# Optimization experiments

Hardware: AMD Instinct MI355X
Metric: run time of the kernel (lower is better)

## Reference

```python
import jax, jax.numpy as jnp
import numpy as np

N = 65536      # num ref nodes
M = 65536      # num query nodes
E = 1572864    # num edges (avg degree 24)
K0 = 27        # num kernels (3x3x3 neighborhood)
D1 = 64        # input channels
D2 = 64        # output channels


def setup_inputs() -> dict:
    key = jax.random.key(0)
    k1, k2, k3, k4, k5, k6 = jax.random.split(key, 6)
    # kernel init mirrors initialize_kernel_weight (uniform in [-bound, bound])
    fan_in = D1 * K0
    gain = float(np.sqrt(2.0 / (1.0 + 5.0)))  # leaky_relu gain with slope sqrt(5)
    std = gain / np.sqrt(fan_in)
    bound = float(np.sqrt(3.0) * std)
    kernel = jax.random.uniform(k1, (K0, D1, D2), minval=-bound, maxval=bound, dtype=jnp.float32)
    ref_feat = jax.random.normal(k2, (N, D1), dtype=jnp.float32)
    e_kernel = jax.random.randint(k3, (E,), 0, K0)
    e_ref = jax.random.randint(k4, (E,), 0, N)
    e_query = jax.random.randint(k5, (E,), 0, M)
    e_weight = jax.random.uniform(k6, (E,), dtype=jnp.float32)
    return {
        "kernel": kernel,
        "ref_feat": ref_feat,
        "e_kernel": e_kernel,
        "e_ref": e_ref,
        "e_query": e_query,
        "num_queries": M,
        "e_weight": e_weight,
    }


def reference(kernel, ref_feat, e_kernel, e_ref, e_query, num_queries, e_weight):
    # Math of MessagePassing.forward:
    #   query_feat[m] = sum_{edges e: e_query[e]==m} w_e * (ref_feat[e_ref[e]] @ kernel[e_kernel[e]])
    # Efficient form: precompute each node's transform under every kernel
    # (N*K0*D1*D2 dense GEMM), then gather per edge and scatter-reduce.
    transformed = jnp.einsum('nd,kdo->nko', ref_feat, kernel)   # [N, K0, D2]
    msgs = transformed[e_ref, e_kernel] * e_weight[:, None]      # [E, D2]
    query_feat = jax.ops.segment_sum(msgs, e_query, num_segments=num_queries)  # [M, D2]
    return query_feat
```

## Files before the change

### kernel.cpp

```cpp
#include <hip/hip_runtime.h>

#define DIN 64
#define DOUT 64
#define MAXK 32

typedef __bf16 bf16x8 __attribute__((ext_vector_type(8)));
typedef float  f32x4  __attribute__((ext_vector_type(4)));
typedef unsigned int u32x4 __attribute__((ext_vector_type(4)));

static __device__ inline unsigned short f2b(float x) {
    return __builtin_bit_cast(unsigned short, (__bf16)x);
}
static __device__ inline float b2f(unsigned short u) {
    return __uint_as_float(((unsigned int)u) << 16);
}


__global__ void conv_w_kernel(const float* __restrict__ W,
                              unsigned short* __restrict__ Wt, int total,
                              int* __restrict__ qcount, int NB) {
    int i = blockIdx.x * blockDim.x + threadIdx.x;
    if (i < NB) qcount[i] = 0;
    if (i < total) {
        int j    = i & 7;
        int lane = (i >> 3) & 63;
        int h    = (i >> 9) & 1;
        int t    = (i >> 10) & 3;
        int k    = i >> 12;
        int col  = lane & 15;
        int quad = lane >> 4;
        int d1 = h * 32 + quad * 8 + j;
        int d2 = t * 16 + col;
        Wt[i] = f2b(W[(k * 64 + d1) * 64 + d2]);
    }
}


#define KSPLIT 8

__global__ __launch_bounds__(256) void phaseA_v3_kernel(
    const float* __restrict__ ref,
    const unsigned short* __restrict__ Wt,
    unsigned short* __restrict__ T,
    int K0, int Nn)
{
    const int lane = threadIdx.x & 63;
    const int wid  = threadIdx.x >> 6;
    const int col  = lane & 15;
    const int quad = lane >> 4;
    const int n0   = blockIdx.x * 64 + wid * 16;
    const int row  = n0 + col;

    const int kch = (K0 + KSPLIT - 1) / KSPLIT;
    const int k0  = blockIdx.y * kch;
    int k1 = k0 + kch;
    if (k1 > K0) k1 = K0;

    __shared__ __align__(16) char ldsbuf[4 * 2 * 2304];
    char* bufs = ldsbuf + wid * 2 * 2304;

    const float* rp = ref + (size_t)row * 64;
    f32x4 r0 = *reinterpret_cast<const f32x4*>(rp + quad * 8);
    f32x4 r1 = *reinterpret_cast<const f32x4*>(rp + quad * 8 + 4);
    f32x4 r2 = *reinterpret_cast<const f32x4*>(rp + 32 + quad * 8);
    f32x4 r3 = *reinterpret_cast<const f32x4*>(rp + 32 + quad * 8 + 4);
    bf16x8 b0, b1;
    #pragma unroll
    for (int i = 0; i < 4; ++i) {
        b0[i]     = (__bf16)r0[i];
        b0[4 + i] = (__bf16)r1[i];
        b1[i]     = (__bf16)r2[i];
        b1[4 + i] = (__bf16)r3[i];
    }

    const int rrow = lane >> 2;
    const int rq   = lane & 3;

    for (int k = k0; k < k1; ++k) {
        char* buf = bufs + (k & 1) * 2304;
        const unsigned short* Wk = Wt + (size_t)k * 4096;
        #pragma unroll
        for (int t = 0; t < 4; ++t) {
            const unsigned short* ap = Wk + (size_t)t * 1024 + lane * 8;
            bf16x8 a0 = *reinterpret_cast<const bf16x8*>(ap);
            bf16x8 a1 = *reinterpret_cast<const bf16x8*>(ap + 512);
            f32x4 c = {0.f, 0.f, 0.f, 0.f};
            c = __builtin_amdgcn_mfma_f32_16x16x32_bf16(a0, b0, c, 0, 0, 0);
            c = __builtin_amdgcn_mfma_f32_16x16x32_bf16(a1, b1, c, 0, 0, 0);
            unsigned int lo = (unsigned int)f2b(c[0]) | ((unsigned int)f2b(c[1]) << 16);
            unsigned int hi = (unsigned int)f2b(c[2]) | ((unsigned int)f2b(c[3]) << 16);
            *reinterpret_cast<uint2*>(buf + col * 144 + t * 32 + quad * 8) =
                make_uint2(lo, hi);
        }
        u32x4 v0 = *reinterpret_cast<const u32x4*>(buf + rrow * 144 + rq * 32);
        u32x4 v1 = *reinterpret_cast<const u32x4*>(buf + rrow * 144 + rq * 32 + 16);
        size_t gbase = ((size_t)k * Nn + n0 + rrow) * 64 + rq * 16;
        *reinterpret_cast<u32x4*>(T + gbase)     = v0;
        *reinterpret_cast<u32x4*>(T + gbase + 8) = v1;
    }
}


__global__ void p1_hist_kernel(const int* __restrict__ eq, int E,
                               int* __restrict__ qcount) {
    __shared__ int l[1024];
    const int t = threadIdx.x;
    #pragma unroll
    for (int s4 = 0; s4 < 4; ++s4) l[t + s4 * 256] = 0;
    __syncthreads();
    int stride = gridDim.x * blockDim.x;
    for (int i = blockIdx.x * blockDim.x + t; i < E; i += stride)
        atomicAdd(&l[((unsigned)eq[i]) >> 6], 1);
    __syncthreads();
    #pragma unroll
    for (int s4 = 0; s4 < 4; ++s4) {
        int v = l[t + s4 * 256];
        if (v) atomicAdd(&qcount[t + s4 * 256], v);
    }
}

__global__ void p1_scan_kernel(const int* __restrict__ qcount,
                               int* __restrict__ gbase, int* __restrict__ gcursor,
                               int* __restrict__ qstart, int NB, int M, int E) {
    __shared__ int sh[1024];
    int t = threadIdx.x;
    int v = (t < NB) ? qcount[t] : 0;
    sh[t] = v;
    __syncthreads();
    #pragma unroll
    for (int o = 1; o < 1024; o <<= 1) {
        int x = (t >= o) ? sh[t - o] : 0;
        __syncthreads();
        sh[t] += x;
        __syncthreads();
    }
    int ex = sh[t] - v;
    if (t < NB) { gbase[t] = ex; gcursor[t] = ex; }
    if (t == 0) qstart[M] = E;
}

__global__ __launch_bounds__(256) void p1_scatter_kernel(
    const int* __restrict__ eq, const int* __restrict__ er,
    const int* __restrict__ ek, const float* __restrict__ ew,
    int E, int* __restrict__ gcursor, uint2* __restrict__ tmp)
{
    __shared__ int bin[1024];
    __shared__ int base[1024];
    const int t = threadIdx.x;
    #pragma unroll
    for (int s4 = 0; s4 < 4; ++s4) bin[t + s4 * 256] = 0;
    __syncthreads();
    const int i0 = blockIdx.x * 4096;
    unsigned key[16];
    unsigned rank[16];
    uint2 pay[16];
    #pragma unroll
    for (int u = 0; u < 16; ++u) {
        int i = i0 + u * 256 + t;
        if (i < E) {
            int q = eq[i];
            unsigned b = ((unsigned)q) >> 6;
            key[u] = b;
            rank[u] = atomicAdd(&bin[b], 1);
            pay[u] = make_uint2((unsigned)er[i] | ((unsigned)ek[i] << 16) |
                                ((unsigned)(q & 63) << 21),
                                __float_as_uint(ew[i]));
        } else {
            key[u] = 0xFFFFFFFFu;
        }
    }
    __syncthreads();
    #pragma unroll
    for (int s4 = 0; s4 < 4; ++s4) {
        int bb = t + s4 * 256;
        int c = bin[bb];
        if (c) base[bb] = atomicAdd(&gcursor[bb], c);
    }
    __syncthreads();
    #pragma unroll
    for (int u = 0; u < 16; ++u) {
        if (key[u] != 0xFFFFFFFFu)
            tmp[(size_t)base[key[u]] + rank[u]] = pay[u];
    }
}

__global__ __launch_bounds__(256) void p2_kernel(
    const uint2* __restrict__ tmp, const int* __restrict__ gbase,
    const int* __restrict__ qcount, uint2* __restrict__ rec,
    int* __restrict__ qstart)
{
    __shared__ int fine[64];
    __shared__ int foff[64];
    const int b = blockIdx.x;
    const int t = threadIdx.x;
    const int s = gbase[b];
    const int L = qcount[b];
    if (t < 64) fine[t] = 0;
    __syncthreads();
    for (int i = t; i < L; i += 256)
        atomicAdd(&fine[(tmp[s + i].x >> 21) & 63], 1);
    __syncthreads();
    if (t < 64) {
        int v = fine[t];
        int x = v;
        #pragma unroll
        for (int o = 1; o < 64; o <<= 1) {
            int y = __shfl_up(x, o);
            if (t >= o) x += y;
        }
        foff[t] = x - v;
        qstart[b * 64 + t] = s + x - v;
        fine[t] = 0;
    }
    __syncthreads();
    for (int i = t; i < L; i += 256) {
        uint2 p = tmp[s + i];
        unsigned fb = (p.x >> 21) & 63;
        int r = atomicAdd(&fine[fb], 1);
        rec[(size_t)s + foff[fb] + r] = p;
    }
}


__global__ __launch_bounds__(256) void phaseB_kernel(
    const unsigned short* __restrict__ T,
    const uint2* __restrict__ rec,
    const int* __restrict__ qstart,
    float* __restrict__ out, int Nn)
{
    const int lane = threadIdx.x & 63;
    const int wid  = threadIdx.x >> 6;
    const int q    = blockIdx.x * 4 + wid;

    int beg = qstart[q];
    int end = qstart[q + 1];
    int cnt = end - beg;
    float acc = 0.f;

    if (cnt <= 64) {
        uint2 rv = make_uint2(0u, 0u);
        if (lane < cnt) rv = rec[beg + lane];
        int j = 0;
        for (; j + 8 <= cnt; j += 8) {
            float partial[8];
            #pragma unroll
            for (int u = 0; u < 8; ++u) {
                unsigned mx = (unsigned)__builtin_amdgcn_readlane((int)rv.x, j + u);
                unsigned mw = (unsigned)__builtin_amdgcn_readlane((int)rv.y, j + u);
                unsigned off = (((mx >> 16) & 31) * (unsigned)Nn + (mx & 0xFFFFu)) * 64u
                               + (unsigned)lane;
                partial[u] = __uint_as_float(mw) * b2f(T[off]);
            }
            #pragma unroll
            for (int u = 0; u < 8; ++u) acc += partial[u];
        }
        for (; j < cnt; ++j) {
            unsigned mx = (unsigned)__builtin_amdgcn_readlane((int)rv.x, j);
            unsigned mw = (unsigned)__builtin_amdgcn_readlane((int)rv.y, j);
            unsigned off = (((mx >> 16) & 31) * (unsigned)Nn + (mx & 0xFFFFu)) * 64u
                           + (unsigned)lane;
            acc = fmaf(__uint_as_float(mw), b2f(T[off]), acc);
        }
    } else {
        for (int j = beg; j < end; ++j) {
            uint2 v0 = rec[j];
            unsigned m0 = __builtin_amdgcn_readfirstlane(v0.x);
            float w0 = __uint_as_float(__builtin_amdgcn_readfirstlane(v0.y));
            unsigned off = (((m0 >> 16) & 31) * (unsigned)Nn + (m0 & 0xFFFFu)) * 64u
                           + (unsigned)lane;
            acc = fmaf(w0, b2f(T[off]), acc);
        }
    }
    out[(size_t)q * 64 + lane] = acc;
}


__global__ void hist_kernel(const int* __restrict__ ek, int E, int* __restrict__ counts) {
    __shared__ int l[MAXK];
    if (threadIdx.x < MAXK) l[threadIdx.x] = 0;
    __syncthreads();
    int stride = gridDim.x * blockDim.x;
    for (int i = blockIdx.x * blockDim.x + threadIdx.x; i < E; i += stride)
        atomicAdd(&l[ek[i]], 1);
    __syncthreads();
    if (threadIdx.x < MAXK) {
        int v = l[threadIdx.x];
        if (v) atomicAdd(&counts[threadIdx.x], v);
    }
}

__global__ void scan_kernel(const int* __restrict__ counts, int K,
                            int* __restrict__ start, int* __restrict__ cursor) {
    if (threadIdx.x == 0 && blockIdx.x == 0) {
        int acc = 0;
        for (int k = 0; k < K; ++k) {
            start[k] = acc;
            cursor[k] = acc;
            acc += counts[k];
        }
    }
}

__global__ void scatter_kernel(const int* __restrict__ ek, int E,
                               int* __restrict__ cursor, int* __restrict__ sorted) {
    __shared__ int lcnt[MAXK], lbase[MAXK], lpos[MAXK];
    if (threadIdx.x < MAXK) { lcnt[threadIdx.x] = 0; lpos[threadIdx.x] = 0; }
    __syncthreads();
    int i = blockIdx.x * blockDim.x + threadIdx.x;
    int k = 0;
    bool valid = (i < E);
    if (valid) { k = ek[i]; atomicAdd(&lcnt[k], 1); }
    __syncthreads();
    if (threadIdx.x < MAXK) {
        int v = lcnt[threadIdx.x];
        if (v) lbase[threadIdx.x] = atomicAdd(&cursor[threadIdx.x], v);
    }
    __syncthreads();
    if (valid) {
        int slot = lbase[k] + atomicAdd(&lpos[k], 1);
        sorted[slot] = i;
    }
}

__global__ __launch_bounds__(256) void mp_bucket_kernel(
    const float* __restrict__ W, const float* __restrict__ ref,
    const int* __restrict__ e_ref, const int* __restrict__ e_query,
    const float* __restrict__ e_weight, const int* __restrict__ sorted,
    const int* __restrict__ start, const int* __restrict__ counts,
    float* __restrict__ out)
{
    const int k = blockIdx.y;
    const int lane = threadIdx.x & 63;
    const int wid = threadIdx.x >> 6;

    float wreg[DIN];
    const float* Wk = W + k * DIN * DOUT;
    #pragma unroll
    for (int d = 0; d < DIN; ++d) wreg[d] = Wk[d * DOUT + lane];

    const int s = start[k];
    const int c = counts[k];
    const int nwaves = gridDim.x * 4;

    for (int i = blockIdx.x * 4 + wid; i < c; i += nwaves) {
        int eid = __builtin_amdgcn_readfirstlane(sorted[s + i]);
        int r = e_ref[eid];
        int q = e_query[eid];
        float w = e_weight[eid];
        const float* row = ref + r * DIN;
        float a0 = 0.f, a1 = 0.f, a2 = 0.f, a3 = 0.f;
        #pragma unroll
        for (int d = 0; d < DIN; d += 4) {
            a0 += row[d + 0] * wreg[d + 0];
            a1 += row[d + 1] * wreg[d + 1];
            a2 += row[d + 2] * wreg[d + 2];
            a3 += row[d + 3] * wreg[d + 3];
        }
        atomicAdd(&out[q * DOUT + lane], ((a0 + a1) + (a2 + a3)) * w);
    }
}


extern "C" void kernel_launch(void* const* d_in, const int* in_sizes, int n_in,
                              void* d_out, int out_size, void* d_ws, size_t ws_size,
                              hipStream_t stream) {
    const float* W        = (const float*)d_in[0];
    const float* ref      = (const float*)d_in[1];
    const int*   e_kernel = (const int*)d_in[2];
    const int*   e_ref    = (const int*)d_in[3];
    const int*   e_query  = (const int*)d_in[4];
    const float* e_weight = (const float*)d_in[6];

    const int K0 = in_sizes[0] / (DIN * DOUT);
    const int N  = in_sizes[1] / DIN;
    const int E  = in_sizes[2];
    const int M  = out_size / DOUT;
    const int KD = K0 * 64;
    const int NB = M / 64;

    float* out = (float*)d_out;

    size_t off = 0;
    auto alloc = [&](size_t bytes, size_t align) {
        off = (off + align - 1) / align * align;
        size_t r = off; off += bytes; return r;
    };
    size_t o_tmp     = alloc((size_t)E * 8, 16);
    size_t o_rec     = alloc((size_t)E * 8, 16);
    size_t o_qstart  = alloc((size_t)(M + 1) * 4, 4);
    size_t o_qcount  = alloc(1024 * 4, 4);
    size_t o_gbase   = alloc(1024 * 4, 4);
    size_t o_gcursor = alloc(1024 * 4, 4);
    size_t o_wt      = alloc((size_t)K0 * 4096 * 2, 16);
    size_t o_T       = alloc((size_t)N * KD * 2, 16);
    size_t needA = off;

    bool planA_ok = (ws_size >= needA) && (M % 64 == 0) && (NB >= 1) && (NB <= 1024) &&
                    (N % 64 == 0) && (N <= 65536) && (K0 <= 32);

    if (planA_ok) {
        char* ws = (char*)d_ws;
        uint2* tmp           = (uint2*)(ws + o_tmp);
        uint2* rec           = (uint2*)(ws + o_rec);
        int*  qstart         = (int*)(ws + o_qstart);
        int*  qcount         = (int*)(ws + o_qcount);
        int*  gbase          = (int*)(ws + o_gbase);
        int*  gcursor        = (int*)(ws + o_gcursor);
        unsigned short* Wt   = (unsigned short*)(ws + o_wt);
        unsigned short* T    = (unsigned short*)(ws + o_T);

        int zgrid = (K0 * 4096 > NB) ? K0 * 4096 : NB;
        conv_w_kernel<<<(zgrid + 255) / 256, 256, 0, stream>>>(W, Wt, K0 * 4096,
                                                               qcount, NB);
        p1_hist_kernel<<<512, 256, 0, stream>>>(e_query, E, qcount);
        p1_scan_kernel<<<1, 1024, 0, stream>>>(qcount, gbase, gcursor, qstart, NB, M, E);
        p1_scatter_kernel<<<(E + 4095) / 4096, 256, 0, stream>>>(e_query, e_ref, e_kernel,
                                                                 e_weight, E, gcursor, tmp);
        p2_kernel<<<NB, 256, 0, stream>>>(tmp, gbase, qcount, rec, qstart);

        dim3 agrid(N / 64, KSPLIT);
        phaseA_v3_kernel<<<agrid, 256, 0, stream>>>(ref, Wt, T, K0, N);

        phaseB_kernel<<<M / 4, 256, 0, stream>>>(T, rec, qstart, out, N);
    } else {
        hipMemsetAsync(out, 0, (size_t)out_size * sizeof(float), stream);
        size_t needB = (size_t)(96 + E) * sizeof(int);
        if (ws_size >= needB) {
            int* ws_i   = (int*)d_ws;
            int* counts = ws_i;
            int* start  = ws_i + 32;
            int* cursor = ws_i + 64;
            int* sorted = ws_i + 96;
            hipMemsetAsync(counts, 0, 96 * sizeof(int), stream);
            hist_kernel<<<512, 256, 0, stream>>>(e_kernel, E, counts);
            scan_kernel<<<1, 64, 0, stream>>>(counts, K0, start, cursor);
            scatter_kernel<<<(E + 255) / 256, 256, 0, stream>>>(e_kernel, E, cursor, sorted);
            dim3 grid(64, K0);
            mp_bucket_kernel<<<grid, 256, 0, stream>>>(W, ref, e_ref, e_query, e_weight,
                                                       sorted, start, counts, out);
        }
    }
}
```

Measured before the change: 287.5 us.

## Fuse preprocessing kernels and accumulate query groups in LDS, dropping fine sort

The separate histogram and weight-conversion kernels are merged into one launch, and the coarse edge scatter is merged with the dense per-kernel transform GEMM into a single heterogeneous grid so the two can run concurrently. The second-level per-query sort (p2) is removed. Instead, phase B processes 128-query buckets per block and accumulates messages into a shared-memory tile with LDS float atomics. This removes a full pass over the edge records and several launches, at the cost of LDS atomic contention and a large 32KB LDS footprint per block that may reduce occupancy.

Result: slower. 700.0 us (+143.5%).

```diff
diff --git a/kernel.cpp b/kernel.cpp
--- a/kernel.cpp
+++ b/kernel.cpp
@@ -3,6 +3,8 @@
 #define DIN 64
 #define DOUT 64
 #define MAXK 32
+#define KSPLIT 8
+#define QG 128
 
 typedef __bf16 bf16x8 __attribute__((ext_vector_type(8)));
 typedef float  f32x4  __attribute__((ext_vector_type(4)));
@@ -16,48 +18,75 @@
 }
 
 
-__global__ void conv_w_kernel(const float* __restrict__ W,
-                              unsigned short* __restrict__ Wt, int total,
-                              int* __restrict__ qcount, int NB) {
-    int i = blockIdx.x * blockDim.x + threadIdx.x;
-    if (i < NB) qcount[i] = 0;
-    if (i < total) {
-        int j    = i & 7;
-        int lane = (i >> 3) & 63;
-        int h    = (i >> 9) & 1;
-        int t    = (i >> 10) & 3;
-        int k    = i >> 12;
-        int col  = lane & 15;
-        int quad = lane >> 4;
-        int d1 = h * 32 + quad * 8 + j;
-        int d2 = t * 16 + col;
-        Wt[i] = f2b(W[(k * 64 + d1) * 64 + d2]);
-    }
-}
-
-
-#define KSPLIT 8
-
-__global__ __launch_bounds__(256) void phaseA_v3_kernel(
+__global__ __launch_bounds__(256) void pre_kernel(
+    const float* __restrict__ W, unsigned short* __restrict__ Wt, int total,
+    const int* __restrict__ eq, int E, int* __restrict__ qcount, int HB)
+{
+    const int t = threadIdx.x;
+    if ((int)blockIdx.x < HB) {
+        __shared__ int l[1024];
+        #pragma unroll
+        for (int s4 = 0; s4 < 4; ++s4) l[t + s4 * 256] = 0;
+        __syncthreads();
+        const int stride = HB * 256;
+        for (int i = (int)blockIdx.x * 256 + t; i < E; i += stride)
+            atomicAdd(&l[((unsigned)eq[i]) >> 7], 1);
+        __syncthreads();
+        #pragma unroll
+        for (int s4 = 0; s4 < 4; ++s4) {
+            int v = l[t + s4 * 256];
+            if (v) atomicAdd(&qcount[t + s4 * 256], v);
+        }
+    } else {
+        int i = ((int)blockIdx.x - HB) * 256 + t;
+        if (i < total) {
+            int j    = i & 7;
+            int lane = (i >> 3) & 63;
+            int h    = (i >> 9) & 1;
+            int tt   = (i >> 10) & 3;
+            int k    = i >> 12;
+            int col  = lane & 15;
+            int quad = lane >> 4;
+            int d1 = h * 32 + quad * 8 + j;
+            int d2 = tt * 16 + col;
+            Wt[i] = f2b(W[(k * 64 + d1) * 64 + d2]);
+        }
+    }
+}
+
+__global__ void p1_scan_kernel(const int* __restrict__ qcount,
+                               int* __restrict__ gbase, int* __restrict__ gcursor,
+                               int NB) {
+    __shared__ int sh[1024];
+    int t = threadIdx.x;
+    int v = (t < NB) ? qcount[t] : 0;
+    sh[t] = v;
+    __syncthreads();
+    #pragma unroll
+    for (int o = 1; o < 1024; o <<= 1) {
+        int x = (t >= o) ? sh[t - o] : 0;
+        __syncthreads();
+        sh[t] += x;
+        __syncthreads();
+    }
+    int ex = sh[t] - v;
+    if (t < NB) { gbase[t] = ex; gcursor[t] = ex; }
+}
+
+
+static __device__ __forceinline__ void phaseA_body(
     const float* __restrict__ ref,
     const unsigned short* __restrict__ Wt,
     unsigned short* __restrict__ T,
-    int K0, int Nn)
+    int K0, int Nn, int nblk, int k0, int k1, char* lds)
 {
     const int lane = threadIdx.x & 63;
     const int wid  = threadIdx.x >> 6;
     const int col  = lane & 15;
     const int quad = lane >> 4;
-    const int n0   = blockIdx.x * 64 + wid * 16;
+    const int n0   = nblk * 64 + wid * 16;
     const int row  = n0 + col;
-
-    const int kch = (K0 + KSPLIT - 1) / KSPLIT;
-    const int k0  = blockIdx.y * kch;
-    int k1 = k0 + kch;
-    if (k1 > K0) k1 = K0;
-
-    __shared__ __align__(16) char ldsbuf[4 * 2 * 2304];
-    char* bufs = ldsbuf + wid * 2 * 2304;
+    char* bufs = lds + wid * 2 * 2304;
 
     const float* rp = ref + (size_t)row * 64;
     f32x4 r0 = *reinterpret_cast<const f32x4*>(rp + quad * 8);
@@ -101,177 +130,124 @@
 }
 
 
-__global__ void p1_hist_kernel(const int* __restrict__ eq, int E,
-                               int* __restrict__ qcount) {
-    __shared__ int l[1024];
-    const int t = threadIdx.x;
-    #pragma unroll
-    for (int s4 = 0; s4 < 4; ++s4) l[t + s4 * 256] = 0;
-    __syncthreads();
-    int stride = gridDim.x * blockDim.x;
-    for (int i = blockIdx.x * blockDim.x + t; i < E; i += stride)
-        atomicAdd(&l[((unsigned)eq[i]) >> 6], 1);
-    __syncthreads();
-    #pragma unroll
-    for (int s4 = 0; s4 < 4; ++s4) {
-        int v = l[t + s4 * 256];
-        if (v) atomicAdd(&qcount[t + s4 * 256], v);
-    }
-}
-
-__global__ void p1_scan_kernel(const int* __restrict__ qcount,
-                               int* __restrict__ gbase, int* __restrict__ gcursor,
-                               int* __restrict__ qstart, int NB, int M, int E) {
-    __shared__ int sh[1024];
-    int t = threadIdx.x;
-    int v = (t < NB) ? qcount[t] : 0;
-    sh[t] = v;
-    __syncthreads();
-    #pragma unroll
-    for (int o = 1; o < 1024; o <<= 1) {
-        int x = (t >= o) ? sh[t - o] : 0;
-        __syncthreads();
-        sh[t] += x;
-        __syncthreads();
-    }
-    int ex = sh[t] - v;
-    if (t < NB) { gbase[t] = ex; gcursor[t] = ex; }
-    if (t == 0) qstart[M] = E;
-}
-
-__global__ __launch_bounds__(256) void p1_scatter_kernel(
+__global__ __launch_bounds__(256) void fusedA_scatter_kernel(
+    const float* __restrict__ ref, const unsigned short* __restrict__ Wt,
+    unsigned short* __restrict__ T, int K0, int Nn, int SCB, int NA,
     const int* __restrict__ eq, const int* __restrict__ er,
     const int* __restrict__ ek, const float* __restrict__ ew,
     int E, int* __restrict__ gcursor, uint2* __restrict__ tmp)
 {
+    __shared__ __align__(16) char ldsbuf[4 * 2 * 2304];
     __shared__ int bin[1024];
     __shared__ int base[1024];
     const int t = threadIdx.x;
-    #pragma unroll
-    for (int s4 = 0; s4 < 4; ++s4) bin[t + s4 * 256] = 0;
-    __syncthreads();
-    const int i0 = blockIdx.x * 4096;
-    unsigned key[16];
-    unsigned rank[16];
-    uint2 pay[16];
-    #pragma unroll
-    for (int u = 0; u < 16; ++u) {
-        int i = i0 + u * 256 + t;
-        if (i < E) {
-            int q = eq[i];
-            unsigned b = ((unsigned)q) >> 6;
-            key[u] = b;
-            rank[u] = atomicAdd(&bin[b], 1);
-            pay[u] = make_uint2((unsigned)er[i] | ((unsigned)ek[i] << 16) |
-                                ((unsigned)(q & 63) << 21),
-                                __float_as_uint(ew[i]));
-        } else {
-            key[u] = 0xFFFFFFFFu;
-        }
-    }
-    __syncthreads();
-    #pragma unroll
-    for (int s4 = 0; s4 < 4; ++s4) {
-        int bb = t + s4 * 256;
-        int c = bin[bb];
-        if (c) base[bb] = atomicAdd(&gcursor[bb], c);
-    }
-    __syncthreads();
-    #pragma unroll
-    for (int u = 0; u < 16; ++u) {
-        if (key[u] != 0xFFFFFFFFu)
-            tmp[(size_t)base[key[u]] + rank[u]] = pay[u];
-    }
-}
-
-__global__ __launch_bounds__(256) void p2_kernel(
-    const uint2* __restrict__ tmp, const int* __restrict__ gbase,
-    const int* __restrict__ qcount, uint2* __restrict__ rec,
-    int* __restrict__ qstart)
-{
-    __shared__ int fine[64];
-    __shared__ int foff[64];
-    const int b = blockIdx.x;
-    const int t = threadIdx.x;
-    const int s = gbase[b];
-    const int L = qcount[b];
-    if (t < 64) fine[t] = 0;
-    __syncthreads();
-    for (int i = t; i < L; i += 256)
-        atomicAdd(&fine[(tmp[s + i].x >> 21) & 63], 1);
-    __syncthreads();
-    if (t < 64) {
-        int v = fine[t];
-        int x = v;
-        #pragma unroll
-        for (int o = 1; o < 64; o <<= 1) {
-            int y = __shfl_up(x, o);
-            if (t >= o) x += y;
-        }
-        foff[t] = x - v;
-        qstart[b * 64 + t] = s + x - v;
-        fine[t] = 0;
-    }
-    __syncthreads();
-    for (int i = t; i < L; i += 256) {
-        uint2 p = tmp[s + i];
-        unsigned fb = (p.x >> 21) & 63;
-        int r = atomicAdd(&fine[fb], 1);
-        rec[(size_t)s + foff[fb] + r] = p;
-    }
-}
-
-
-__global__ __launch_bounds__(256) void phaseB_kernel(
+
+    if ((int)blockIdx.x < SCB) {
+        #pragma unroll
+        for (int s4 = 0; s4 < 4; ++s4) bin[t + s4 * 256] = 0;
+        __syncthreads();
+        const int i0 = (int)blockIdx.x * 4096;
+        unsigned key[16];
+        unsigned rank[16];
+        uint2 pay[16];
+        #pragma unroll
+        for (int u = 0; u < 16; ++u) {
+            int i = i0 + u * 256 + t;
+            if (i < E) {
+                int q = eq[i];
+                unsigned b = ((unsigned)q) >> 7;
+                key[u] = b;
+                rank[u] = atomicAdd(&bin[b], 1);
+                pay[u] = make_uint2((unsigned)er[i] | ((unsigned)ek[i] << 16) |
+                                    ((unsigned)(q & (QG - 1)) << 21),
+                                    __float_as_uint(ew[i]));
+            } else {
+                key[u] = 0xFFFFFFFFu;
+            }
+        }
+        __syncthreads();
+        #pragma unroll
+        for (int s4 = 0; s4 < 4; ++s4) {
+            int bb = t + s4 * 256;
+            int c = bin[bb];
+            if (c) base[bb] = atomicAdd(&gcursor[bb], c);
+        }
+        __syncthreads();
+        #pragma unroll
+        for (int u = 0; u < 16; ++u) {
+            if (key[u] != 0xFFFFFFFFu)
+                tmp[(size_t)base[key[u]] + rank[u]] = pay[u];
+        }
+    } else {
+        const int ab   = (int)blockIdx.x - SCB;
+        const int nblk = ab % NA;
+        const int ky   = ab / NA;
+        const int kch  = (K0 + KSPLIT - 1) / KSPLIT;
+        const int k0   = ky * kch;
+        if (k0 >= K0) return;
+        int k1 = k0 + kch;
+        if (k1 > K0) k1 = K0;
+        phaseA_body(ref, Wt, T, K0, Nn, nblk, k0, k1, ldsbuf);
+    }
+}
+
+
+__global__ __launch_bounds__(512) void phaseB2_kernel(
     const unsigned short* __restrict__ T,
-    const uint2* __restrict__ rec,
-    const int* __restrict__ qstart,
+    const uint2* __restrict__ tmp,
+    const int* __restrict__ gbase, const int* __restrict__ qcount,
     float* __restrict__ out, int Nn)
 {
-    const int lane = threadIdx.x & 63;
-    const int wid  = threadIdx.x >> 6;
-    const int q    = blockIdx.x * 4 + wid;
-
-    int beg = qstart[q];
-    int end = qstart[q + 1];
-    int cnt = end - beg;
-    float acc = 0.f;
-
-    if (cnt <= 64) {
-        uint2 rv = make_uint2(0u, 0u);
-        if (lane < cnt) rv = rec[beg + lane];
-        int j = 0;
-        for (; j + 8 <= cnt; j += 8) {
-            float partial[8];
-            #pragma unroll
-            for (int u = 0; u < 8; ++u) {
-                unsigned mx = (unsigned)__builtin_amdgcn_readlane((int)rv.x, j + u);
-                unsigned mw = (unsigned)__builtin_amdgcn_readlane((int)rv.y, j + u);
-                unsigned off = (((mx >> 16) & 31) * (unsigned)Nn + (mx & 0xFFFFu)) * 64u
-                               + (unsigned)lane;
-                partial[u] = __uint_as_float(mw) * b2f(T[off]);
-            }
-            #pragma unroll
-            for (int u = 0; u < 8; ++u) acc += partial[u];
-        }
-        for (; j < cnt; ++j) {
-            unsigned mx = (unsigned)__builtin_amdgcn_readlane((int)rv.x, j);
-            unsigned mw = (unsigned)__builtin_amdgcn_readlane((int)rv.y, j);
+    __shared__ float acc[QG * 64];
+    const int t    = threadIdx.x;
+    const int lane = t & 63;
+    const int wid  = t >> 6;
+    const int b    = blockIdx.x;
+
+    #pragma unroll
+    for (int i = 0; i < (QG * 64) / 512; ++i) acc[t + i * 512] = 0.f;
+    __syncthreads();
+
+    const int s   = gbase[b];
+    const int L   = qcount[b];
+    const int end = s + L;
+    const int G   = L >> 3;
+
+    for (int g = wid; g < G; g += 8) {
+        const int j0 = s + g * 8;
+        float partial[8];
+        int   qv[8];
+        #pragma unroll
+        for (int u = 0; u < 8; ++u) {
+            uint2 v = tmp[j0 + u];
+            unsigned mx = (unsigned)__builtin_amdgcn_readfirstlane((int)v.x);
+            unsigned mw = (unsigned)__builtin_amdgcn_readfirstlane((int)v.y);
             unsigned off = (((mx >> 16) & 31) * (unsigned)Nn + (mx & 0xFFFFu)) * 64u
                            + (unsigned)lane;
-            acc = fmaf(__uint_as_float(mw), b2f(T[off]), acc);
-        }
-    } else {
-        for (int j = beg; j < end; ++j) {
-            uint2 v0 = rec[j];
-            unsigned m0 = __builtin_amdgcn_readfirstlane(v0.x);
-            float w0 = __uint_as_float(__builtin_amdgcn_readfirstlane(v0.y));
-            unsigned off = (((m0 >> 16) & 31) * (unsigned)Nn + (m0 & 0xFFFFu)) * 64u
+            partial[u] = __uint_as_float(mw) * b2f(T[off]);
+            qv[u] = (int)((mx >> 21) & (QG - 1));
+        }
+        #pragma unroll
+        for (int u = 0; u < 8; ++u)
+            atomicAdd(&acc[qv[u] * 64 + lane], partial[u]);
+    }
+    if (wid == 0) {
+        for (int j = s + (G << 3); j < end; ++j) {
+            uint2 v = tmp[j];
+            unsigned mx = (unsigned)__builtin_amdgcn_readfirstlane((int)v.x);
+            unsigned mw = (unsigned)__builtin_amdgcn_readfirstlane((int)v.y);
+            unsigned off = (((mx >> 16) & 31) * (unsigned)Nn + (mx & 0xFFFFu)) * 64u
                            + (unsigned)lane;
-            acc = fmaf(w0, b2f(T[off]), acc);
-        }
-    }
-    out[(size_t)q * 64 + lane] = acc;
+            atomicAdd(&acc[(int)((mx >> 21) & (QG - 1)) * 64 + lane],
+                      __uint_as_float(mw) * b2f(T[off]));
+        }
+    }
+    __syncthreads();
+
+    const size_t ob = (size_t)b * QG * 64;
+    #pragma unroll
+    for (int i = 0; i < (QG * 64) / 512; ++i)
+        out[ob + t + i * 512] = acc[t + i * 512];
 }
 
 
@@ -376,7 +352,7 @@
     const int E  = in_sizes[2];
     const int M  = out_size / DOUT;
     const int KD = K0 * 64;
-    const int NB = M / 64;
+    const int NB = M / QG;
 
     float* out = (float*)d_out;
 
@@ -386,8 +362,6 @@
         size_t r = off; off += bytes; return r;
     };
     size_t o_tmp     = alloc((size_t)E * 8, 16);
-    size_t o_rec     = alloc((size_t)E * 8, 16);
-    size_t o_qstart  = alloc((size_t)(M + 1) * 4, 4);
     size_t o_qcount  = alloc(1024 * 4, 4);
     size_t o_gbase   = alloc(1024 * 4, 4);
     size_t o_gcursor = alloc(1024 * 4, 4);
@@ -395,33 +369,35 @@
     size_t o_T       = alloc((size_t)N * KD * 2, 16);
     size_t needA = off;
 
-    bool planA_ok = (ws_size >= needA) && (M % 64 == 0) && (NB >= 1) && (NB <= 1024) &&
+    bool planA_ok = (ws_size >= needA) && (M % QG == 0) && (NB >= 1) && (NB <= 1024) &&
                     (N % 64 == 0) && (N <= 65536) && (K0 <= 32);
 
     if (planA_ok) {
         char* ws = (char*)d_ws;
         uint2* tmp           = (uint2*)(ws + o_tmp);
-        uint2* rec           = (uint2*)(ws + o_rec);
-        int*  qstart         = (int*)(ws + o_qstart);
         int*  qcount         = (int*)(ws + o_qcount);
         int*  gbase          = (int*)(ws + o_gbase);
         int*  gcursor        = (int*)(ws + o_gcursor);
         unsigned short* Wt   = (unsigned short*)(ws + o_wt);
         unsigned short* T    = (unsigned short*)(ws + o_T);
 
-        int zgrid = (K0 * 4096 > NB) ? K0 * 4096 : NB;
-        conv_w_kernel<<<(zgrid + 255) / 256, 256, 0, stream>>>(W, Wt, K0 * 4096,
-                                                               qcount, NB);
-        p1_hist_kernel<<<512, 256, 0, stream>>>(e_query, E, qcount);
-        p1_scan_kernel<<<1, 1024, 0, stream>>>(qcount, gbase, gcursor, qstart, NB, M, E);
-        p1_scatter_kernel<<<(E + 4095) / 4096, 256, 0, stream>>>(e_query, e_ref, e_kernel,
-                                                                 e_weight, E, gcursor, tmp);
-        p2_kernel<<<NB, 256, 0, stream>>>(tmp, gbase, qcount, rec, qstart);
-
-        dim3 agrid(N / 64, KSPLIT);
-        phaseA_v3_kernel<<<agrid, 256, 0, stream>>>(ref, Wt, T, K0, N);
-
-        phaseB_kernel<<<M / 4, 256, 0, stream>>>(T, rec, qstart, out, N);
+        const int HB   = 512;
+        const int CWB  = (K0 * 4096 + 255) / 256;
+        const int SCB  = (E + 4095) / 4096;
+        const int NA   = N / 64;
+
+        hipMemsetAsync(qcount, 0, 1024 * sizeof(int), stream);
+
+        pre_kernel<<<HB + CWB, 256, 0, stream>>>(W, Wt, K0 * 4096,
+                                                 e_query, E, qcount, HB);
+
+        p1_scan_kernel<<<1, 1024, 0, stream>>>(qcount, gbase, gcursor, NB);
+
+        fusedA_scatter_kernel<<<SCB + NA * KSPLIT, 256, 0, stream>>>(
+            ref, Wt, T, K0, N, SCB, NA,
+            e_query, e_ref, e_kernel, e_weight, E, gcursor, tmp);
+
+        phaseB2_kernel<<<NB, 512, 0, stream>>>(T, tmp, gbase, qcount, out, N);
     } else {
         hipMemsetAsync(out, 0, (size_t)out_size * sizeof(float), stream);
         size_t needB = (size_t)(96 + E) * sizeof(int);
```

## Co-schedule phase-A GEMM blocks with edge scatter and bucket-sort kernels

Applied to the files above, without the earlier changes.

The dense per-kernel transform (phase A) is split into two slices of the kernel index range. The first slice runs as extra blocks inside the coarse edge-scatter kernel, the second inside the fine bucket-sort kernel, so the compute-bound MFMA work overlaps the memory- and atomic-bound sorting passes instead of running as its own launch. The histogram and weight conversion are merged into one launch, and coarse query buckets grow from 64 to 128 queries with 1024-thread blocks. The trade-off is larger blocks with bigger LDS footprints, a single LDS staging buffer per wave, and a fixed split constant (KS4) that may balance the two kernels poorly.

After: 274.9 us. -4.4%, faster.

```diff
diff --git a/kernel.cpp b/kernel.cpp
--- a/kernel.cpp
+++ b/kernel.cpp
@@ -3,6 +3,9 @@
 #define DIN 64
 #define DOUT 64
 #define MAXK 32
+#define KSPLIT 8
+#define KS4 5
+#define QG 128
 
 typedef __bf16 bf16x8 __attribute__((ext_vector_type(8)));
 typedef float  f32x4  __attribute__((ext_vector_type(4)));
@@ -15,49 +18,73 @@
     return __uint_as_float(((unsigned int)u) << 16);
 }
 
-
-__global__ void conv_w_kernel(const float* __restrict__ W,
-                              unsigned short* __restrict__ Wt, int total,
-                              int* __restrict__ qcount, int NB) {
-    int i = blockIdx.x * blockDim.x + threadIdx.x;
-    if (i < NB) qcount[i] = 0;
-    if (i < total) {
-        int j    = i & 7;
-        int lane = (i >> 3) & 63;
-        int h    = (i >> 9) & 1;
-        int t    = (i >> 10) & 3;
-        int k    = i >> 12;
-        int col  = lane & 15;
-        int quad = lane >> 4;
-        int d1 = h * 32 + quad * 8 + j;
-        int d2 = t * 16 + col;
-        Wt[i] = f2b(W[(k * 64 + d1) * 64 + d2]);
-    }
-}
-
-
-#define KSPLIT 8
-
-__global__ __launch_bounds__(256) void phaseA_v3_kernel(
+__global__ __launch_bounds__(256) void pre_kernel(
+    const float* __restrict__ W, unsigned short* __restrict__ Wt, int total,
+    const int* __restrict__ eq, int E, int* __restrict__ qcount, int HB)
+{
+    const int t = threadIdx.x;
+    if ((int)blockIdx.x < HB) {
+        __shared__ int l[512];
+        l[t] = 0; l[t + 256] = 0;
+        __syncthreads();
+        const int stride = HB * 256;
+        for (int i = (int)blockIdx.x * 256 + t; i < E; i += stride)
+            atomicAdd(&l[((unsigned)eq[i]) >> 7], 1);
+        __syncthreads();
+        int v0 = l[t];       if (v0) atomicAdd(&qcount[t], v0);
+        int v1 = l[t + 256]; if (v1) atomicAdd(&qcount[t + 256], v1);
+    } else {
+        int i = ((int)blockIdx.x - HB) * 256 + t;
+        if (i < total) {
+            int j    = i & 7;
+            int lane = (i >> 3) & 63;
+            int h    = (i >> 9) & 1;
+            int tt   = (i >> 10) & 3;
+            int k    = i >> 12;
+            int col  = lane & 15;
+            int quad = lane >> 4;
+            int d1 = h * 32 + quad * 8 + j;
+            int d2 = tt * 16 + col;
+            Wt[i] = f2b(W[(k * 64 + d1) * 64 + d2]);
+        }
+    }
+}
+
+__global__ void p1_scan_kernel(const int* __restrict__ qcount,
+                               int* __restrict__ gbase, int* __restrict__ gcursor,
+                               int* __restrict__ qstart, int NB, int M, int E) {
+    __shared__ int sh[1024];
+    int t = threadIdx.x;
+    int v = (t < NB) ? qcount[t] : 0;
+    sh[t] = v;
+    __syncthreads();
+    #pragma unroll
+    for (int o = 1; o < 1024; o <<= 1) {
+        int x = (t >= o) ? sh[t - o] : 0;
+        __syncthreads();
+        sh[t] += x;
+        __syncthreads();
+    }
+    int ex = sh[t] - v;
+    if (t < NB) { gbase[t] = ex; gcursor[t] = ex; }
+    if (t == 0) qstart[M] = E;
+}
+
+
+static __device__ __forceinline__ void phaseA_body16(
     const float* __restrict__ ref,
     const unsigned short* __restrict__ Wt,
     unsigned short* __restrict__ T,
-    int K0, int Nn)
-{
-    const int lane = threadIdx.x & 63;
-    const int wid  = threadIdx.x >> 6;
+    int K0, int Nn, int nblk, int k0, int k1, char* lds)
+{
+    const int t    = threadIdx.x;
+    const int lane = t & 63;
+    const int wid  = t >> 6;
     const int col  = lane & 15;
     const int quad = lane >> 4;
-    const int n0   = blockIdx.x * 64 + wid * 16;
+    const int n0   = nblk * 256 + wid * 16;
     const int row  = n0 + col;
-
-    const int kch = (K0 + KSPLIT - 1) / KSPLIT;
-    const int k0  = blockIdx.y * kch;
-    int k1 = k0 + kch;
-    if (k1 > K0) k1 = K0;
-
-    __shared__ __align__(16) char ldsbuf[4 * 2 * 2304];
-    char* bufs = ldsbuf + wid * 2 * 2304;
+    char* buf = lds + wid * 2304;
 
     const float* rp = ref + (size_t)row * 64;
     f32x4 r0 = *reinterpret_cast<const f32x4*>(rp + quad * 8);
@@ -77,11 +104,10 @@
     const int rq   = lane & 3;
 
     for (int k = k0; k < k1; ++k) {
-        char* buf = bufs + (k & 1) * 2304;
         const unsigned short* Wk = Wt + (size_t)k * 4096;
         #pragma unroll
-        for (int t = 0; t < 4; ++t) {
-            const unsigned short* ap = Wk + (size_t)t * 1024 + lane * 8;
+        for (int tt = 0; tt < 4; ++tt) {
+            const unsigned short* ap = Wk + (size_t)tt * 1024 + lane * 8;
             bf16x8 a0 = *reinterpret_cast<const bf16x8*>(ap);
             bf16x8 a1 = *reinterpret_cast<const bf16x8*>(ap + 512);
             f32x4 c = {0.f, 0.f, 0.f, 0.f};
@@ -89,135 +115,130 @@
             c = __builtin_amdgcn_mfma_f32_16x16x32_bf16(a1, b1, c, 0, 0, 0);
             unsigned int lo = (unsigned int)f2b(c[0]) | ((unsigned int)f2b(c[1]) << 16);
             unsigned int hi = (unsigned int)f2b(c[2]) | ((unsigned int)f2b(c[3]) << 16);
-            *reinterpret_cast<uint2*>(buf + col * 144 + t * 32 + quad * 8) =
+            *reinterpret_cast<uint2*>(buf + col * 144 + tt * 32 + quad * 8) =
                 make_uint2(lo, hi);
         }
         u32x4 v0 = *reinterpret_cast<const u32x4*>(buf + rrow * 144 + rq * 32);
         u32x4 v1 = *reinterpret_cast<const u32x4*>(buf + rrow * 144 + rq * 32 + 16);
-        size_t gbase = ((size_t)k * Nn + n0 + rrow) * 64 + rq * 16;
-        *reinterpret_cast<u32x4*>(T + gbase)     = v0;
-        *reinterpret_cast<u32x4*>(T + gbase + 8) = v1;
-    }
-}
-
-
-__global__ void p1_hist_kernel(const int* __restrict__ eq, int E,
-                               int* __restrict__ qcount) {
-    __shared__ int l[1024];
-    const int t = threadIdx.x;
-    #pragma unroll
-    for (int s4 = 0; s4 < 4; ++s4) l[t + s4 * 256] = 0;
-    __syncthreads();
-    int stride = gridDim.x * blockDim.x;
-    for (int i = blockIdx.x * blockDim.x + t; i < E; i += stride)
-        atomicAdd(&l[((unsigned)eq[i]) >> 6], 1);
-    __syncthreads();
-    #pragma unroll
-    for (int s4 = 0; s4 < 4; ++s4) {
-        int v = l[t + s4 * 256];
-        if (v) atomicAdd(&qcount[t + s4 * 256], v);
-    }
-}
-
-__global__ void p1_scan_kernel(const int* __restrict__ qcount,
-                               int* __restrict__ gbase, int* __restrict__ gcursor,
-                               int* __restrict__ qstart, int NB, int M, int E) {
-    __shared__ int sh[1024];
-    int t = threadIdx.x;
-    int v = (t < NB) ? qcount[t] : 0;
-    sh[t] = v;
-    __syncthreads();
-    #pragma unroll
-    for (int o = 1; o < 1024; o <<= 1) {
-        int x = (t >= o) ? sh[t - o] : 0;
-        __syncthreads();
-        sh[t] += x;
-        __syncthreads();
-    }
-    int ex = sh[t] - v;
-    if (t < NB) { gbase[t] = ex; gcursor[t] = ex; }
-    if (t == 0) qstart[M] = E;
-}
-
-__global__ __launch_bounds__(256) void p1_scatter_kernel(
+        size_t gb = ((size_t)k * Nn + n0 + rrow) * 64 + rq * 16;
+        *reinterpret_cast<u32x4*>(T + gb)     = v0;
+        *reinterpret_cast<u32x4*>(T + gb + 8) = v1;
+    }
+}
+
+
+__global__ __launch_bounds__(1024) void fusedA_scatter_kernel(
+    const float* __restrict__ ref, const unsigned short* __restrict__ Wt,
+    unsigned short* __restrict__ T, int K0, int Nn, int SCB, int NA2,
     const int* __restrict__ eq, const int* __restrict__ er,
     const int* __restrict__ ek, const float* __restrict__ ew,
     int E, int* __restrict__ gcursor, uint2* __restrict__ tmp)
 {
-    __shared__ int bin[1024];
-    __shared__ int base[1024];
+    __shared__ __align__(16) char ldsbuf[16 * 2304];
+    __shared__ int bin[512];
+    __shared__ int base[512];
     const int t = threadIdx.x;
-    #pragma unroll
-    for (int s4 = 0; s4 < 4; ++s4) bin[t + s4 * 256] = 0;
-    __syncthreads();
-    const int i0 = blockIdx.x * 4096;
-    unsigned key[16];
-    unsigned rank[16];
-    uint2 pay[16];
-    #pragma unroll
-    for (int u = 0; u < 16; ++u) {
-        int i = i0 + u * 256 + t;
-        if (i < E) {
-            int q = eq[i];
-            unsigned b = ((unsigned)q) >> 6;
-            key[u] = b;
-            rank[u] = atomicAdd(&bin[b], 1);
-            pay[u] = make_uint2((unsigned)er[i] | ((unsigned)ek[i] << 16) |
-                                ((unsigned)(q & 63) << 21),
-                                __float_as_uint(ew[i]));
-        } else {
-            key[u] = 0xFFFFFFFFu;
-        }
-    }
-    __syncthreads();
-    #pragma unroll
-    for (int s4 = 0; s4 < 4; ++s4) {
-        int bb = t + s4 * 256;
-        int c = bin[bb];
-        if (c) base[bb] = atomicAdd(&gcursor[bb], c);
-    }
-    __syncthreads();
-    #pragma unroll
-    for (int u = 0; u < 16; ++u) {
-        if (key[u] != 0xFFFFFFFFu)
-            tmp[(size_t)base[key[u]] + rank[u]] = pay[u];
-    }
-}
-
-__global__ __launch_bounds__(256) void p2_kernel(
+
+    if ((int)blockIdx.x < SCB) {
+        if (t < 512) bin[t] = 0;
+        __syncthreads();
+        const int i0 = (int)blockIdx.x * 8192;
+        unsigned key[8];
+        unsigned rank[8];
+        uint2 pay[8];
+        #pragma unroll
+        for (int u = 0; u < 8; ++u) {
+            int i = i0 + u * 1024 + t;
+            if (i < E) {
+                int q = eq[i];
+                unsigned b = ((unsigned)q) >> 7;
+                key[u] = b;
+                rank[u] = atomicAdd(&bin[b], 1);
+                pay[u] = make_uint2((unsigned)er[i] | ((unsigned)ek[i] << 16) |
+                                    ((unsigned)(q & (QG - 1)) << 21),
+                                    __float_as_uint(ew[i]));
+            } else {
+                key[u] = 0xFFFFFFFFu;
+            }
+        }
+        __syncthreads();
+        if (t < 512) {
+            int c = bin[t];
+            if (c) base[t] = atomicAdd(&gcursor[t], c);
+        }
+        __syncthreads();
+        #pragma unroll
+        for (int u = 0; u < 8; ++u) {
+            if (key[u] != 0xFFFFFFFFu)
+                tmp[(size_t)base[key[u]] + rank[u]] = pay[u];
+        }
+    } else {
+        const int ab   = (int)blockIdx.x - SCB;
+        const int nblk = ab % NA2;
+        const int ky   = ab / NA2;
+        const int kch  = (K0 + KSPLIT - 1) / KSPLIT;
+        const int k0   = ky * kch;
+        if (k0 >= K0) return;
+        int k1 = k0 + kch;
+        if (k1 > K0) k1 = K0;
+        phaseA_body16(ref, Wt, T, K0, Nn, nblk, k0, k1, ldsbuf);
+    }
+}
+
+__global__ __launch_bounds__(1024) void fusedA_p2_kernel(
+    const float* __restrict__ ref, const unsigned short* __restrict__ Wt,
+    unsigned short* __restrict__ T, int K0, int Nn, int NB, int NA2,
     const uint2* __restrict__ tmp, const int* __restrict__ gbase,
     const int* __restrict__ qcount, uint2* __restrict__ rec,
     int* __restrict__ qstart)
 {
-    __shared__ int fine[64];
-    __shared__ int foff[64];
-    const int b = blockIdx.x;
+    __shared__ __align__(16) char ldsbuf[16 * 2304];
+    __shared__ int fine[QG];
+    __shared__ int foff[QG];
+    __shared__ int vsave[QG];
     const int t = threadIdx.x;
-    const int s = gbase[b];
-    const int L = qcount[b];
-    if (t < 64) fine[t] = 0;
-    __syncthreads();
-    for (int i = t; i < L; i += 256)
-        atomicAdd(&fine[(tmp[s + i].x >> 21) & 63], 1);
-    __syncthreads();
-    if (t < 64) {
-        int v = fine[t];
-        int x = v;
+
+    if ((int)blockIdx.x < NB) {
+        const int b = (int)blockIdx.x;
+        const int s = gbase[b];
+        const int L = qcount[b];
+        if (t < QG) fine[t] = 0;
+        __syncthreads();
+        for (int i = t; i < L; i += 1024)
+            atomicAdd(&fine[(tmp[s + i].x >> 21) & (QG - 1)], 1);
+        __syncthreads();
+        if (t < QG) vsave[t] = fine[t];
+        __syncthreads();
         #pragma unroll
-        for (int o = 1; o < 64; o <<= 1) {
-            int y = __shfl_up(x, o);
-            if (t >= o) x += y;
-        }
-        foff[t] = x - v;
-        qstart[b * 64 + t] = s + x - v;
-        fine[t] = 0;
-    }
-    __syncthreads();
-    for (int i = t; i < L; i += 256) {
-        uint2 p = tmp[s + i];
-        unsigned fb = (p.x >> 21) & 63;
-        int r = atomicAdd(&fine[fb], 1);
-        rec[(size_t)s + foff[fb] + r] = p;
+        for (int o = 1; o < QG; o <<= 1) {
+            int x = (t >= o && t < QG) ? fine[t - o] : 0;
+            __syncthreads();
+            if (t < QG) fine[t] += x;
+            __syncthreads();
+        }
+        if (t < QG) {
+            int ex = fine[t] - vsave[t];
+            foff[t] = ex;
+            qstart[b * QG + t] = s + ex;
+            fine[t] = 0;
+        }
+        __syncthreads();
+        for (int i = t; i < L; i += 1024) {
+            uint2 p = tmp[s + i];
+            unsigned fb = (p.x >> 21) & (QG - 1);
+            int r = atomicAdd(&fine[fb], 1);
+            rec[(size_t)s + foff[fb] + r] = p;
+        }
+    } else {
+        const int ab   = (int)blockIdx.x - NB;
+        const int nblk = ab % NA2;
+        const int ky   = KS4 + ab / NA2;
+        const int kch  = (K0 + KSPLIT - 1) / KSPLIT;
+        const int k0   = ky * kch;
+        if (k0 >= K0) return;
+        int k1 = k0 + kch;
+        if (k1 > K0) k1 = K0;
+        phaseA_body16(ref, Wt, T, K0, Nn, nblk, k0, k1, ldsbuf);
     }
 }
 
@@ -376,7 +397,7 @@
     const int E  = in_sizes[2];
     const int M  = out_size / DOUT;
     const int KD = K0 * 64;
-    const int NB = M / 64;
+    const int NB = M / QG;
 
     float* out = (float*)d_out;
 
@@ -395,8 +416,8 @@
     size_t o_T       = alloc((size_t)N * KD * 2, 16);
     size_t needA = off;
 
-    bool planA_ok = (ws_size >= needA) && (M % 64 == 0) && (NB >= 1) && (NB <= 1024) &&
-                    (N % 64 == 0) && (N <= 65536) && (K0 <= 32);
+    bool planA_ok = (ws_size >= needA) && (M % QG == 0) && (NB >= 1) && (NB <= 512) &&
+                    (N % 256 == 0) && (N <= 65536) && (K0 <= 32);
 
     if (planA_ok) {
         char* ws = (char*)d_ws;
@@ -409,17 +430,25 @@
         unsigned short* Wt   = (unsigned short*)(ws + o_wt);
         unsigned short* T    = (unsigned short*)(ws + o_T);
 
-        int zgrid = (K0 * 4096 > NB) ? K0 * 4096 : NB;
-        conv_w_kernel<<<(zgrid + 255) / 256, 256, 0, stream>>>(W, Wt, K0 * 4096,
-                                                               qcount, NB);
-        p1_hist_kernel<<<512, 256, 0, stream>>>(e_query, E, qcount);
+        const int HB   = 512;
+        const int CWB  = (K0 * 4096 + 255) / 256;
+        const int SCB  = (E + 8191) / 8192;
+        const int NA2  = N / 256;
+
+        hipMemsetAsync(qcount, 0, 1024 * sizeof(int), stream);
+
+        pre_kernel<<<HB + CWB, 256, 0, stream>>>(W, Wt, K0 * 4096,
+                                                 e_query, E, qcount, HB);
+
         p1_scan_kernel<<<1, 1024, 0, stream>>>(qcount, gbase, gcursor, qstart, NB, M, E);
-        p1_scatter_kernel<<<(E + 4095) / 4096, 256, 0, stream>>>(e_query, e_ref, e_kernel,
-                                                                 e_weight, E, gcursor, tmp);
-        p2_kernel<<<NB, 256, 0, stream>>>(tmp, gbase, qcount, rec, qstart);
-
-        dim3 agrid(N / 64, KSPLIT);
-        phaseA_v3_kernel<<<agrid, 256, 0, stream>>>(ref, Wt, T, K0, N);
+
+        fusedA_scatter_kernel<<<SCB + NA2 * KS4, 1024, 0, stream>>>(
+            ref, Wt, T, K0, N, SCB, NA2,
+            e_query, e_ref, e_kernel, e_weight, E, gcursor, tmp);
+
+        fusedA_p2_kernel<<<NB + NA2 * (KSPLIT - KS4), 1024, 0, stream>>>(
+            ref, Wt, T, K0, N, NB, NA2,
+            tmp, gbase, qcount, rec, qstart);
 
         phaseB_kernel<<<M / 4, 256, 0, stream>>>(T, rec, qstart, out, N);
     } else {
```
